# Kernel tuning notes

Hardware: AMD Instinct MI355X
Metric: run time of the kernel (lower is better)

The kernel has to match this reference:

```python
import jax, jax.numpy as jnp
import numpy as np

N = 8192
D_IN = 128
D_HID = 256  # hard-coded nn.Linear(input_dim, 256) in the module
D_OUT = 64
BN_EPS = 1e-5
LEAKY_SLOPE = 0.01


def setup_inputs() -> dict:
    key = jax.random.key(0)
    k_h, k_a, k_wt, k_wo = jax.random.split(key, 4)
    H = jax.random.normal(k_h, (N, D_IN), dtype=jnp.float32)
    # Fixed adjacency passed to __init__; values in [0,1) so mask=ceil(A*1e-5) is {0,1}
    A = jax.random.uniform(k_a, (N, N), dtype=jnp.float32)
    bn_weight = jnp.ones((D_IN,), jnp.float32)
    bn_bias = jnp.zeros((D_IN,), jnp.float32)
    W_theta = jax.random.normal(k_wt, (D_IN, D_HID), jnp.float32) * np.float32(1.0 / np.sqrt(D_IN))
    b_theta = jnp.zeros((D_HID,), jnp.float32)
    W_out = jax.random.normal(k_wo, (D_IN, D_OUT), jnp.float32) * np.float32(1.0 / np.sqrt(D_IN))
    b_out = jnp.zeros((D_OUT,), jnp.float32)
    return {"H": H, "A": A, "bn_weight": bn_weight, "bn_bias": bn_bias,
            "W_theta": W_theta, "b_theta": b_theta, "W_out": W_out, "b_out": b_out}


def reference(H, A, bn_weight, bn_bias, W_theta, b_theta, W_out, b_out):
    # BatchNorm1d in training mode: biased batch statistics over the node dim
    mean = jnp.mean(H, axis=0)
    var = jnp.mean(jnp.square(H - mean), axis=0)
    Hn = (H - mean) * jax.lax.rsqrt(var + BN_EPS) * bn_weight + bn_bias  # [N, D_IN]

    Hx = Hn @ W_theta + b_theta  # [N, 256]
    mask = jnp.ceil(A * 1e-5)    # constant {0,1} mask from fixed adjacency

    # Dynamic adjacency: clamp(sigmoid(Hx Hx^T), min=0.1) * mask + I
    S = jnp.clip(jax.nn.sigmoid(Hx @ Hx.T), 0.1, None)  # [N, N]
    Ad = S * mask + jnp.eye(N, dtype=H.dtype)

    # D^{-1/2} A D^{-1/2} via broadcast scaling (same math as diag matmuls)
    d = jax.lax.rsqrt(jnp.sum(Ad, axis=1))  # D^{-0.5}, [N]
    A_hat = Ad * d[:, None] * d[None, :]

    out = A_hat @ (Hn @ W_out + b_out)       # [N, D_OUT]
    out = jnp.where(out >= 0, out, LEAKY_SLOPE * out)  # LeakyReLU(0.01)
    return out, A_hat
```

## Files before the change

kernel.cpp:

```cpp
#include <hip/hip_runtime.h>
#include <hip/hip_bf16.h>

#define N 8192
#define DIN 128
#define DHID 256
#define DOUT 64
#define LDP 72

typedef __attribute__((ext_vector_type(8))) short short8;
typedef __attribute__((ext_vector_type(4))) float f32x4;
typedef __attribute__((ext_vector_type(4))) unsigned short u16x4;

__device__ inline unsigned short f2bf(float x) {
  unsigned u = __float_as_uint(x);
  u += 0x7FFF + ((u >> 16) & 1);
  return (unsigned short)(u >> 16);
}
__device__ inline float bf2f(unsigned short u) {
  return __uint_as_float(((unsigned)u) << 16);
}
__device__ inline float sig_clip(float x) {
  float s = 1.0f / (1.0f + __expf(-x));
  return fmaxf(s, 0.1f);
}

__global__ void bn_stats(const float* __restrict__ H, const float* __restrict__ bnw,
                         const float* __restrict__ bnb, float* __restrict__ scale,
                         float* __restrict__ shift) {
  int f = blockIdx.x;
  int t = threadIdx.x;
  float s = 0.f, sq = 0.f;
  for (int r = t; r < N; r += 256) {
    float v = H[(size_t)r * DIN + f];
    s += v; sq += v * v;
  }
  __shared__ float ss[256], s2[256];
  ss[t] = s; s2[t] = sq;
  __syncthreads();
  for (int o = 128; o > 0; o >>= 1) {
    if (t < o) { ss[t] += ss[t + o]; s2[t] += s2[t + o]; }
    __syncthreads();
  }
  if (t == 0) {
    float mean = ss[0] * (1.0f / N);
    float var = s2[0] * (1.0f / N) - mean * mean;
    float sc = rsqrtf(var + 1e-5f) * bnw[f];
    scale[f] = sc;
    shift[f] = bnb[f] - mean * sc;
  }
}

__global__ __launch_bounds__(256) void proj(const float* __restrict__ H,
                     const float* __restrict__ scale, const float* __restrict__ shift,
                     const float* __restrict__ Wt, const float* __restrict__ bt,
                     const float* __restrict__ Wo, const float* __restrict__ bo,
                     unsigned short* __restrict__ Hx, unsigned short* __restrict__ M2) {
  __shared__ float hn[8][DIN];
  int i0 = blockIdx.x * 8;
  int t = threadIdx.x;
  #pragma unroll
  for (int rep = 0; rep < 4; ++rep) {
    int idx = rep * 256 + t;
    int r = idx >> 7, c = idx & 127;
    float h = H[(size_t)(i0 + r) * DIN + c];
    hn[r][c] = fmaf(h, scale[c], shift[c]);
  }
  __syncthreads();
  {
    int c = t;
    float acc[8];
    float b = bt[c];
    #pragma unroll
    for (int r = 0; r < 8; ++r) acc[r] = b;
    for (int k = 0; k < DIN; ++k) {
      float w = Wt[k * DHID + c];
      #pragma unroll
      for (int r = 0; r < 8; ++r) acc[r] = fmaf(hn[r][k], w, acc[r]);
    }
    #pragma unroll
    for (int r = 0; r < 8; ++r) Hx[(size_t)(i0 + r) * DHID + c] = f2bf(acc[r]);
  }
  if (t < DOUT) {
    int c = t;
    float acc[8];
    float b = bo[c];
    #pragma unroll
    for (int r = 0; r < 8; ++r) acc[r] = b;
    for (int k = 0; k < DIN; ++k) {
      float w = Wo[k * DOUT + c];
      #pragma unroll
      for (int r = 0; r < 8; ++r) acc[r] = fmaf(hn[r][k], w, acc[r]);
    }
    #pragma unroll
    for (int r = 0; r < 8; ++r) M2[(size_t)(i0 + r) * DOUT + c] = f2bf(acc[r]);
  }
}

template <int BF16V>
__global__ __launch_bounds__(256) void smat(const unsigned short* __restrict__ Hx,
                     const float* __restrict__ A,
                     float* __restrict__ rowsum,
                     void* __restrict__ Vout) {
  __shared__ unsigned short la[128][LDP];
  __shared__ unsigned short lb[128][LDP];
  int jt = blockIdx.x, it = blockIdx.y;
  int i0 = it * 128, j0 = jt * 128;
  int t = threadIdx.x;
  int w = t >> 6, l = t & 63;
  int lr = l & 15, lg = l >> 4;

  unsigned um[2] = {0u, 0u};
  #pragma unroll
  for (int m = 0; m < 2; ++m) {
    #pragma unroll
    for (int r = 0; r < 4; ++r) {
      int gi = i0 + w * 32 + m * 16 + lg * 4 + r;
      const float* Arow = &A[(size_t)gi * N + j0 + lr];
      #pragma unroll
      for (int n = 0; n < 8; ++n) {
        float a = Arow[n * 16];
        um[m] |= (a > 0.f ? 1u : 0u) << (r * 8 + n);
      }
    }
  }

  f32x4 acc[2][8];
  f32x4 zero = {0.f, 0.f, 0.f, 0.f};
  #pragma unroll
  for (int m = 0; m < 2; ++m)
    #pragma unroll
    for (int n = 0; n < 8; ++n) acc[m][n] = zero;

  for (int c4 = 0; c4 < 4; ++c4) {
    int k0 = c4 * 64;
    __syncthreads();
    #pragma unroll
    for (int rp = 0; rp < 4; ++rp) {
      int row = rp * 32 + (t >> 3);
      int ch = (t & 7) * 8;
      *(short8*)&la[row][ch] = *(const short8*)&Hx[(size_t)(i0 + row) * DHID + k0 + ch];
      *(short8*)&lb[row][ch] = *(const short8*)&Hx[(size_t)(j0 + row) * DHID + k0 + ch];
    }
    __syncthreads();
    #pragma unroll
    for (int kk = 0; kk < 2; ++kk) {
      short8 af[2], bf[8];
      #pragma unroll
      for (int m = 0; m < 2; ++m)
        af[m] = *(const short8*)&la[w * 32 + m * 16 + lr][kk * 32 + lg * 8];
      #pragma unroll
      for (int n = 0; n < 8; ++n)
        bf[n] = *(const short8*)&lb[n * 16 + lr][kk * 32 + lg * 8];
      #pragma unroll
      for (int m = 0; m < 2; ++m)
        #pragma unroll
        for (int n = 0; n < 8; ++n)
          acc[m][n] = __builtin_amdgcn_mfma_f32_16x16x32_bf16(af[m], bf[n], acc[m][n], 0, 0, 0);
    }
  }

  #pragma unroll
  for (int m = 0; m < 2; ++m) {
    #pragma unroll
    for (int r = 0; r < 4; ++r) {
      int gi = i0 + w * 32 + m * 16 + lg * 4 + r;
      float part = 0.f;
      #pragma unroll
      for (int n = 0; n < 8; ++n) {
        int gj = j0 + n * 16 + lr;
        float ms = ((um[m] >> (r * 8 + n)) & 1u) ? 1.f : 0.f;
        float v = sig_clip(acc[m][n][r]) * ms + (gi == gj ? 1.f : 0.f);
        part += v;
        if (BF16V)
          ((unsigned short*)Vout)[(size_t)gi * N + gj] = f2bf(v);
        else
          ((float*)Vout)[(size_t)gi * N + gj] = v;
      }
      part += __shfl_xor(part, 1);
      part += __shfl_xor(part, 2);
      part += __shfl_xor(part, 4);
      part += __shfl_xor(part, 8);
      if (lr == 0) atomicAdd(&rowsum[gi], part);
    }
  }
}

__global__ void dfin(float* rs) {
  int i = blockIdx.x * 256 + threadIdx.x;
  if (i < N) rs[i] = rsqrtf(rs[i]);
}

template <int BF16V>
__global__ __launch_bounds__(256) void outmm(const void* __restrict__ Vin,
                      const float* __restrict__ dd,
                      const unsigned short* __restrict__ M2,
                      float* __restrict__ Ahat, float* __restrict__ out) {
  __shared__ unsigned short la[128][LDP];
  __shared__ unsigned short lbT[64][LDP];
  int kc = blockIdx.x;
  int it = blockIdx.y;
  int i0 = it * 128;
  int jbase = kc * 1024;
  int t = threadIdx.x;
  int w = t >> 6, l = t & 63;
  int lr = l & 15, lg = l >> 4;

  f32x4 acc[2][4];
  f32x4 zero = {0.f, 0.f, 0.f, 0.f};
  #pragma unroll
  for (int m = 0; m < 2; ++m)
    #pragma unroll
    for (int n = 0; n < 4; ++n) acc[m][n] = zero;

  for (int s = 0; s < 16; ++s) {
    int j0 = jbase + s * 64;
    __syncthreads();
    #pragma unroll
    for (int rep = 0; rep < 8; ++rep) {
      int row = rep * 16 + (t >> 4);
      int cc = (t & 15) * 4;
      size_t idx = (size_t)(i0 + row) * N + j0 + cc;
      f32x4 v;
      if (BF16V) {
        u16x4 u = *(const u16x4*)&((const unsigned short*)Vin)[idx];
        v[0] = bf2f(u[0]); v[1] = bf2f(u[1]); v[2] = bf2f(u[2]); v[3] = bf2f(u[3]);
      } else {
        v = *(const f32x4*)&((const float*)Vin)[idx];
      }
      float di = dd[i0 + row];
      f32x4 dj = *(const f32x4*)&dd[j0 + cc];
      f32x4 sv;
      sv[0] = v[0] * di * dj[0]; sv[1] = v[1] * di * dj[1];
      sv[2] = v[2] * di * dj[2]; sv[3] = v[3] * di * dj[3];
      *(f32x4*)&Ahat[idx] = sv;
      u16x4 b;
      b[0] = f2bf(sv[0]); b[1] = f2bf(sv[1]); b[2] = f2bf(sv[2]); b[3] = f2bf(sv[3]);
      *(u16x4*)&la[row][cc] = b;
    }
    #pragma unroll
    for (int rep = 0; rep < 2; ++rep) {
      int idx = rep * 256 + t;
      int row = idx >> 3;
      int ch = (idx & 7) * 8;
      short8 v = *(const short8*)&M2[(size_t)(j0 + row) * DOUT + ch];
      #pragma unroll
      for (int e = 0; e < 8; ++e) lbT[ch + e][row] = (unsigned short)v[e];
    }
    __syncthreads();
    #pragma unroll
    for (int kk = 0; kk < 2; ++kk) {
      short8 af[2], bf[4];
      #pragma unroll
      for (int m = 0; m < 2; ++m)
        af[m] = *(const short8*)&la[w * 32 + m * 16 + lr][kk * 32 + lg * 8];
      #pragma unroll
      for (int n = 0; n < 4; ++n)
        bf[n] = *(const short8*)&lbT[n * 16 + lr][kk * 32 + lg * 8];
      #pragma unroll
      for (int m = 0; m < 2; ++m)
        #pragma unroll
        for (int n = 0; n < 4; ++n)
          acc[m][n] = __builtin_amdgcn_mfma_f32_16x16x32_bf16(af[m], bf[n], acc[m][n], 0, 0, 0);
    }
  }
  #pragma unroll
  for (int m = 0; m < 2; ++m)
    #pragma unroll
    for (int n = 0; n < 4; ++n)
      #pragma unroll
      for (int r = 0; r < 4; ++r) {
        int gi = i0 + w * 32 + m * 16 + lg * 4 + r;
        int gc = n * 16 + lr;
        atomicAdd(&out[(size_t)gi * DOUT + gc], acc[m][n][r]);
      }
}

__global__ void leaky(float* out) {
  int i = blockIdx.x * 256 + threadIdx.x;
  if (i < N * DOUT) {
    float x = out[i];
    out[i] = x >= 0.f ? x : 0.01f * x;
  }
}

extern "C" void kernel_launch(void* const* d_in, const int* in_sizes, int n_in,
                              void* d_out, int out_size, void* d_ws, size_t ws_size,
                              hipStream_t stream) {
  const float* H   = (const float*)d_in[0];
  const float* A   = (const float*)d_in[1];
  const float* bnw = (const float*)d_in[2];
  const float* bnb = (const float*)d_in[3];
  const float* Wt  = (const float*)d_in[4];
  const float* bt  = (const float*)d_in[5];
  const float* Wo  = (const float*)d_in[6];
  const float* bo  = (const float*)d_in[7];
  float* out = (float*)d_out;
  float* Ahat = out + (size_t)N * DOUT;

  char* ws = (char*)d_ws;
  float* scale  = (float*)(ws + 0);
  float* shift  = (float*)(ws + 512);
  float* rowsum = (float*)(ws + 4096);
  unsigned short* M2 = (unsigned short*)(ws + 65536);
  unsigned short* Hx = (unsigned short*)(ws + 2097152);
  unsigned short* Vbf = (unsigned short*)(ws + (size_t)(8u << 20));

  const size_t need_bf16 = (size_t)(8u << 20) + (size_t)N * N * 2;
  const bool big = ws_size >= need_bf16;

  hipMemsetAsync(rowsum, 0, N * sizeof(float), stream);
  hipMemsetAsync(out, 0, (size_t)N * DOUT * sizeof(float), stream);

  bn_stats<<<DIN, 256, 0, stream>>>(H, bnw, bnb, scale, shift);
  proj<<<N / 8, 256, 0, stream>>>(H, scale, shift, Wt, bt, Wo, bo, Hx, M2);
  if (big) {
    smat<1><<<dim3(64, 64), 256, 0, stream>>>(Hx, A, rowsum, (void*)Vbf);
    dfin<<<N / 256, 256, 0, stream>>>(rowsum);
    outmm<1><<<dim3(8, 64), 256, 0, stream>>>((const void*)Vbf, rowsum, M2, Ahat, out);
  } else {
    smat<0><<<dim3(64, 64), 256, 0, stream>>>(Hx, A, rowsum, (void*)Ahat);
    dfin<<<N / 256, 256, 0, stream>>>(rowsum);
    outmm<0><<<dim3(8, 64), 256, 0, stream>>>((const void*)Ahat, rowsum, M2, Ahat, out);
  }
  leaky<<<(N * DOUT + 255) / 256, 256, 0, stream>>>(out);
}
```

Before: 377.2 us.

## Coalesce mask loads via ballot, store M2 transposed, split outmm K twice

The smat mask read now has each wave read contiguous 64-float row segments and packs them into 64-bit masks with ballot, kept in shared memory, instead of scattered strided per-lane loads. proj writes M2 transposed so outmm can load B fragments straight from global memory, which removes the LDS transpose staging. outmm's K range per block is halved so the grid doubles, at the cost of more atomic adds into out. The direct global B-fragment loads may cost latency compared with reading from LDS.

```diff
diff --git a/kernel.cpp b/kernel.cpp
--- a/kernel.cpp
+++ b/kernel.cpp
@@ -54,7 +54,7 @@
                      const float* __restrict__ scale, const float* __restrict__ shift,
                      const float* __restrict__ Wt, const float* __restrict__ bt,
                      const float* __restrict__ Wo, const float* __restrict__ bo,
-                     unsigned short* __restrict__ Hx, unsigned short* __restrict__ M2) {
+                     unsigned short* __restrict__ Hx, unsigned short* __restrict__ M2T) {
   __shared__ float hn[8][DIN];
   int i0 = blockIdx.x * 8;
   int t = threadIdx.x;
@@ -92,7 +92,7 @@
       for (int r = 0; r < 8; ++r) acc[r] = fmaf(hn[r][k], w, acc[r]);
     }
     #pragma unroll
-    for (int r = 0; r < 8; ++r) M2[(size_t)(i0 + r) * DOUT + c] = f2bf(acc[r]);
+    for (int r = 0; r < 8; ++r) M2T[(size_t)c * N + i0 + r] = f2bf(acc[r]);
   }
 }
 
@@ -103,25 +103,22 @@
                      void* __restrict__ Vout) {
   __shared__ unsigned short la[128][LDP];
   __shared__ unsigned short lb[128][LDP];
+  __shared__ unsigned long long mbt[128][2];
   int jt = blockIdx.x, it = blockIdx.y;
   int i0 = it * 128, j0 = jt * 128;
   int t = threadIdx.x;
   int w = t >> 6, l = t & 63;
   int lr = l & 15, lg = l >> 4;
 
-  unsigned um[2] = {0u, 0u};
-  #pragma unroll
-  for (int m = 0; m < 2; ++m) {
-    #pragma unroll
-    for (int r = 0; r < 4; ++r) {
-      int gi = i0 + w * 32 + m * 16 + lg * 4 + r;
-      const float* Arow = &A[(size_t)gi * N + j0 + lr];
-      #pragma unroll
-      for (int n = 0; n < 8; ++n) {
-        float a = Arow[n * 16];
-        um[m] |= (a > 0.f ? 1u : 0u) << (r * 8 + n);
-      }
-    }
+  #pragma unroll 4
+  for (int rr = 0; rr < 32; ++rr) {
+    int row = w * 32 + rr;
+    const float* Arow = &A[(size_t)(i0 + row) * N + j0 + l];
+    float a0 = Arow[0];
+    float a1 = Arow[64];
+    unsigned long long b0 = __ballot(a0 > 0.f);
+    unsigned long long b1 = __ballot(a1 > 0.f);
+    if (l == 0) { mbt[row][0] = b0; mbt[row][1] = b1; }
   }
 
   f32x4 acc[2][8];
@@ -163,12 +160,15 @@
   for (int m = 0; m < 2; ++m) {
     #pragma unroll
     for (int r = 0; r < 4; ++r) {
-      int gi = i0 + w * 32 + m * 16 + lg * 4 + r;
+      int rl = w * 32 + m * 16 + lg * 4 + r;
+      int gi = i0 + rl;
+      unsigned long long w0 = mbt[rl][0], w1 = mbt[rl][1];
       float part = 0.f;
       #pragma unroll
       for (int n = 0; n < 8; ++n) {
         int gj = j0 + n * 16 + lr;
-        float ms = ((um[m] >> (r * 8 + n)) & 1u) ? 1.f : 0.f;
+        int b = n * 16 + lr;
+        float ms = (((n < 4 ? w0 : w1) >> (b & 63)) & 1ull) ? 1.f : 0.f;
         float v = sig_clip(acc[m][n][r]) * ms + (gi == gj ? 1.f : 0.f);
         part += v;
         if (BF16V)
@@ -193,14 +193,13 @@
 template <int BF16V>
 __global__ __launch_bounds__(256) void outmm(const void* __restrict__ Vin,
                       const float* __restrict__ dd,
-                      const unsigned short* __restrict__ M2,
+                      const unsigned short* __restrict__ M2T,
                       float* __restrict__ Ahat, float* __restrict__ out) {
   __shared__ unsigned short la[128][LDP];
-  __shared__ unsigned short lbT[64][LDP];
   int kc = blockIdx.x;
   int it = blockIdx.y;
   int i0 = it * 128;
-  int jbase = kc * 1024;
+  int jbase = kc * 512;
   int t = threadIdx.x;
   int w = t >> 6, l = t & 63;
   int lr = l & 15, lg = l >> 4;
@@ -212,7 +211,7 @@
     #pragma unroll
     for (int n = 0; n < 4; ++n) acc[m][n] = zero;
 
-  for (int s = 0; s < 16; ++s) {
+  for (int s = 0; s < 8; ++s) {
     int j0 = jbase + s * 64;
     __syncthreads();
     #pragma unroll
@@ -237,30 +236,21 @@
       b[0] = f2bf(sv[0]); b[1] = f2bf(sv[1]); b[2] = f2bf(sv[2]); b[3] = f2bf(sv[3]);
       *(u16x4*)&la[row][cc] = b;
     }
-    #pragma unroll
-    for (int rep = 0; rep < 2; ++rep) {
-      int idx = rep * 256 + t;
-      int row = idx >> 3;
-      int ch = (idx & 7) * 8;
-      short8 v = *(const short8*)&M2[(size_t)(j0 + row) * DOUT + ch];
-      #pragma unroll
-      for (int e = 0; e < 8; ++e) lbT[ch + e][row] = (unsigned short)v[e];
-    }
     __syncthreads();
     #pragma unroll
     for (int kk = 0; kk < 2; ++kk) {
-      short8 af[2], bf[4];
+      short8 af[2], bfr[4];
       #pragma unroll
       for (int m = 0; m < 2; ++m)
         af[m] = *(const short8*)&la[w * 32 + m * 16 + lr][kk * 32 + lg * 8];
       #pragma unroll
       for (int n = 0; n < 4; ++n)
-        bf[n] = *(const short8*)&lbT[n * 16 + lr][kk * 32 + lg * 8];
+        bfr[n] = *(const short8*)&M2T[(size_t)(n * 16 + lr) * N + j0 + kk * 32 + lg * 8];
       #pragma unroll
       for (int m = 0; m < 2; ++m)
         #pragma unroll
         for (int n = 0; n < 4; ++n)
-          acc[m][n] = __builtin_amdgcn_mfma_f32_16x16x32_bf16(af[m], bf[n], acc[m][n], 0, 0, 0);
+          acc[m][n] = __builtin_amdgcn_mfma_f32_16x16x32_bf16(af[m], bfr[n], acc[m][n], 0, 0, 0);
     }
   }
   #pragma unroll
@@ -301,8 +291,8 @@
   float* scale  = (float*)(ws + 0);
   float* shift  = (float*)(ws + 512);
   float* rowsum = (float*)(ws + 4096);
-  unsigned short* M2 = (unsigned short*)(ws + 65536);
-  unsigned short* Hx = (unsigned short*)(ws + 2097152);
+  unsigned short* M2T = (unsigned short*)(ws + 65536);
+  unsigned short* Hx  = (unsigned short*)(ws + 2097152);
   unsigned short* Vbf = (unsigned short*)(ws + (size_t)(8u << 20));
 
   const size_t need_bf16 = (size_t)(8u << 20) + (size_t)N * N * 2;
@@ -312,15 +302,15 @@
   hipMemsetAsync(out, 0, (size_t)N * DOUT * sizeof(float), stream);
 
   bn_stats<<<DIN, 256, 0, stream>>>(H, bnw, bnb, scale, shift);
-  proj<<<N / 8, 256, 0, stream>>>(H, scale, shift, Wt, bt, Wo, bo, Hx, M2);
+  proj<<<N / 8, 256, 0, stream>>>(H, scale, shift, Wt, bt, Wo, bo, Hx, M2T);
   if (big) {
     smat<1><<<dim3(64, 64), 256, 0, stream>>>(Hx, A, rowsum, (void*)Vbf);
     dfin<<<N / 256, 256, 0, stream>>>(rowsum);
-    outmm<1><<<dim3(8, 64), 256, 0, stream>>>((const void*)Vbf, rowsum, M2, Ahat, out);
+    outmm<1><<<dim3(16, 64), 256, 0, stream>>>((const void*)Vbf, rowsum, M2T, Ahat, out);
   } else {
     smat<0><<<dim3(64, 64), 256, 0, stream>>>(Hx, A, rowsum, (void*)Ahat);
     dfin<<<N / 256, 256, 0, stream>>>(rowsum);
-    outmm<0><<<dim3(8, 64), 256, 0, stream>>>((const void*)Ahat, rowsum, M2, Ahat, out);
+    outmm<0><<<dim3(16, 64), 256, 0, stream>>>((const void*)Ahat, rowsum, M2T, Ahat, out);
   }
   leaky<<<(N * DOUT + 255) / 256, 256, 0, stream>>>(out);
 }
```

After: 451.8 us. 1.2x slower.
